# Kernel tuning notes

Hardware: AMD Instinct MI355X
Metric: run time of the kernel (lower is better)

Reference implementation:

```python
import jax, jax.numpy as jnp
import numpy as np

D = 512      # Config.vector_sizes[1]
S = 1024     # Config.sequence_lengths[1]
B = 16       # read batch
Q = 64       # Config.use_pndb1
NDOCS = 8    # external A-matrix memory slots
NL = 2       # encoder layers


def rope(x):
    # rotary position embedding over last dim, x: [b, s, d]
    s, d = x.shape[-2], x.shape[-1]
    inv = 1.0 / (10000.0 ** (jnp.arange(0, d, 2, dtype=jnp.float32) / d))
    ang = jnp.arange(s, dtype=jnp.float32)[:, None] * inv[None, :]  # [s, d/2]
    sin, cos = jnp.sin(ang), jnp.cos(ang)
    x1, x2 = x[..., ::2], x[..., 1::2]
    out = jnp.stack([x1 * cos - x2 * sin, x1 * sin + x2 * cos], axis=-1)
    return out.reshape(x.shape)


def layer_norm(x, g, b):
    m = x.mean(-1, keepdims=True)
    v = ((x - m) ** 2).mean(-1, keepdims=True)
    return (x - m) / jnp.sqrt(v + 1e-5) * g + b


def encoder(x, bias, Wqkv, bqkv, Wo, bo, ln, Wff, bff):
    # post-norm transformer encoder, 1 head, rotary on q/k, additive key bias
    d = x.shape[-1]
    scale = 1.0 / jnp.sqrt(jnp.float32(d))
    for l in range(NL):
        q = rope(x @ Wqkv[l, 0] + bqkv[l, 0])
        k = rope(x @ Wqkv[l, 1] + bqkv[l, 1])
        v = x @ Wqkv[l, 2] + bqkv[l, 2]
        scores = jnp.einsum('bqd,bkd->bqk', q, k) * scale + bias[:, None, :]
        a = jax.nn.softmax(scores, axis=-1)
        o = jnp.einsum('bqk,bkd->bqd', a, v) @ Wo[l] + bo[l]
        x = layer_norm(x + o, ln[l, 0, 0], ln[l, 0, 1])
        f = jax.nn.gelu(x @ Wff[l, 0] + bff[l, 0]) @ Wff[l, 1] + bff[l, 1]
        x = layer_norm(x + f, ln[l, 1, 0], ln[l, 1, 1])
    return x


def setup_inputs() -> dict:
    key = jax.random.key(0)
    ks = jax.random.split(key, 24)
    def n(k, shape, s=0.02):
        return jax.random.normal(k, shape, jnp.float32) * s
    ln_init = jnp.tile(jnp.stack([jnp.ones(D), jnp.zeros(D)]), (NL, 2, 1, 1))  # [NL,2,2,D]
    return {
        'raw_emb': jax.random.normal(ks[0], (NDOCS, S, D), jnp.float32),
        'real_pos_write': jax.random.uniform(ks[1], (NDOCS, S), jnp.float32, 0.05, 0.95),
        'post_dec': jax.random.normal(ks[2], (B, S, D), jnp.float32),
        'real_pos_read': jax.random.uniform(ks[4], (B, S), jnp.float32, 0.05, 0.95),
        'questions': jax.random.uniform(ks[5], (Q, D), jnp.float32),
        'W_k': n(ks[6], (D, D)),
        'W_ig': n(ks[7], (D, 1)), 'b_ig': jnp.zeros((1,)),
        'W_u1': n(ks[8], (D, 1)), 'b_u1': jnp.zeros((1,)),
        'W_u2': n(ks[9], (D, 1)), 'b_u2': jnp.zeros((1,)),
        'b1': jax.random.uniform(ks[10], (1,), jnp.float32),
        'W_ok': n(ks[11], (D, D)), 'b_ok': jnp.zeros((D,)),
        'encw_Wqkv': n(ks[12], (NL, 3, D, D)), 'encw_bqkv': jnp.zeros((NL, 3, D)),
        'encw_Wo': n(ks[13], (NL, D, D)), 'encw_bo': jnp.zeros((NL, D)),
        'encw_ln': ln_init,
        'encw_Wff': n(ks[14], (NL, 2, D, D)), 'encw_bff': jnp.zeros((NL, 2, D)),
        'encr_Wqkv': n(ks[15], (NL, 3, D, D)), 'encr_bqkv': jnp.zeros((NL, 3, D)),
        'encr_Wo': n(ks[16], (NL, D, D)), 'encr_bo': jnp.zeros((NL, D)),
        'encr_ln': ln_init,
        'encr_Wff': n(ks[17], (NL, 2, D, D)), 'encr_bff': jnp.zeros((NL, 2, D)),
        'lookup_ids': jax.random.randint(ks[3], (B,), 0, NDOCS, jnp.int32),
    }


def reference(raw_emb, real_pos_write, post_dec, real_pos_read, questions,
              W_k, W_ig, b_ig, W_u1, b_u1, W_u2, b_u2, b1, W_ok, b_ok,
              encw_Wqkv, encw_bqkv, encw_Wo, encw_bo, encw_ln, encw_Wff, encw_bff,
              encr_Wqkv, encr_bqkv, encr_Wo, encr_bo, encr_ln, encr_Wff, encr_bff,
              lookup_ids):
    # ---- create_A_matrix (write path), one A per document ----
    log_pw = jnp.log(real_pos_write)                       # additive key mask
    k = raw_emb @ W_k                                      # to_k (no bias)
    for_ignore = encoder(raw_emb, log_pw, encw_Wqkv, encw_bqkv, encw_Wo,
                         encw_bo, encw_ln, encw_Wff, encw_bff)
    v = raw_emb * jax.nn.sigmoid(for_ignore @ W_ig + b_ig)  # ignore gate
    scores = jnp.einsum('qd,nsd->nqs', questions, k) / jnp.sqrt(jnp.float32(D))
    scores = scores + log_pw[:, None, :]
    A1s = jnp.einsum('nqs,nsd->nqd', jax.nn.softmax(scores, -1), v)  # [NDOCS,Q,D]

    # ---- get_data_from_A_matrix (read path) ----
    logit_pr = jnp.log(real_pos_read) - jnp.log1p(-real_pos_read)  # prob_to_logit
    for_update = encoder(post_dec, logit_pr, encr_Wqkv, encr_bqkv, encr_Wo,
                         encr_bo, encr_ln, encr_Wff, encr_bff)
    k2 = post_dec @ W_ok + b_ok                            # to_output_k
    selA = A1s[lookup_ids]                                 # index_select gather [B,Q,D]
    a2 = jax.nn.softmax(jnp.einsum('bsd,qd->bsq', k2, questions)
                        / jnp.sqrt(jnp.float32(Q)), -1)
    A2 = jnp.einsum('bsq,bqd->bsd', a2, selA)              # [B,S,D]
    gate = jax.nn.sigmoid(for_update @ W_u1 + b_u1 + A2 @ W_u2 + b_u2 + b1 - 4.0)
    out = post_dec * (1.0 - gate) + A2 * gate
    return out, gate
```

## Files before the change

kernel.cpp:

```cpp
#include <hip/hip_runtime.h>
#include <hip/hip_bf16.h>
#include <math.h>

typedef __attribute__((ext_vector_type(8))) short short8;
typedef __attribute__((ext_vector_type(4))) float f32x4;
typedef unsigned short ushortT;

__device__ __forceinline__ unsigned short f2b(float f) {
  union { float f; unsigned u; } v; v.f = f;
  return (unsigned short)((v.u + 0x7FFFu + ((v.u >> 16) & 1u)) >> 16);
}
__device__ __forceinline__ float b2f(unsigned short h) {
  union { unsigned u; float f; } v; v.u = ((unsigned)h) << 16;
  return v.f;
}
__device__ __forceinline__ float gelu_f(float x) {
  return 0.5f * x * (1.0f + tanhf(0.7978845608028654f * (x + 0.044715f * x * x * x)));
}

__device__ __forceinline__ void async16(ushortT* lds, const ushortT* g) {
  __builtin_amdgcn_global_load_lds(
      (const __attribute__((address_space(1))) void*)g,
      (__attribute__((address_space(3))) void*)lds, 16, 0, 0);
}

template<int EMODE>
__global__ __launch_bounds__(256, 3)
void gemm_f(const ushortT* __restrict__ A, const ushortT* __restrict__ Bt,
            const ushortT* __restrict__ A2, const ushortT* __restrict__ Bt2,
            ushortT* __restrict__ C, ushortT* __restrict__ C2,
            const float* __restrict__ bias, const float* __restrict__ bias2,
            int zsplit, int bmode, float scale, long bstride,
            int K, int lda, int ldb, int ldc,
            long sA, long sB, long sC, const float2* __restrict__ tab)
{
  __shared__ ushortT lds[3][2][128 * 32];
  const int gx = gridDim.x, gy = gridDim.y;
  int flat = blockIdx.x + gx * (blockIdx.y + gy * blockIdx.z);
  const int nwg = gx * gy * gridDim.z;
  if ((nwg & 7) == 0) {
    const int per = nwg >> 3;
    flat = (flat & 7) * per + (flat >> 3);
  }
  const int gxy = gx * gy;
  const int z = flat / gxy;
  const int rem = flat - z * gxy;
  const int bm = (rem / gx) * 128, bn = (rem % gx) * 128;

  int zz = z;
  const ushortT* Ap = A; const ushortT* Bp = Bt; const float* bp = bias;
  if (z >= zsplit) { Ap = A2; Bp = Bt2; bp = bias2; zz = z - zsplit; }
  Ap += (long)zz * sA;
  Bp += (long)zz * sB;
  const long coff = (long)z * sC;
  const int tid = threadIdx.x, wave = tid >> 6, lane = tid & 63;
  const int wm = (wave >> 1) << 6, wn = (wave & 1) << 6;
  const int l15 = lane & 15, quad = lane >> 4;

  const ushortT* gA[2]; const ushortT* gB[2];
  int lchunk[2];
#pragma unroll
  for (int q = 0; q < 2; ++q) {
    int r = 32 * wave + 16 * q + (lane >> 2);
    int sw = (((lane & 3) ^ ((r >> 1) & 3)) << 3);
    gA[q] = Ap + (long)(bm + r) * lda + sw;
    gB[q] = Bp + (long)(bn + r) * ldb + sw;
    lchunk[q] = (wave * 2 + q) * 512;
  }

  f32x4 acc[4][4];
#pragma unroll
  for (int i = 0; i < 4; ++i)
#pragma unroll
    for (int j = 0; j < 4; ++j) acc[i][j] = (f32x4){0.f, 0.f, 0.f, 0.f};

  const int x0 = (l15 >> 1) & 3;
  const int nk = K >> 5;

#pragma unroll
  for (int q = 0; q < 2; ++q) {
    async16(&lds[0][0][lchunk[q]], gA[q]);
    async16(&lds[0][1][lchunk[q]], gB[q]);
  }
#pragma unroll
  for (int q = 0; q < 2; ++q) {
    async16(&lds[1][0][lchunk[q]], gA[q] + 32);
    async16(&lds[1][1][lchunk[q]], gB[q] + 32);
  }

  int rb_ = 0, sb_ = 2;
  for (int k = 0; k < nk; ++k) {
    if (k + 2 < nk) {
      int k0 = (k + 2) << 5;
#pragma unroll
      for (int q = 0; q < 2; ++q) {
        async16(&lds[sb_][0][lchunk[q]], gA[q] + k0);
        async16(&lds[sb_][1][lchunk[q]], gB[q] + k0);
      }
    }
    if (k + 2 < nk)      asm volatile("s_waitcnt vmcnt(8)" ::: "memory");
    else if (k + 1 < nk) asm volatile("s_waitcnt vmcnt(4)" ::: "memory");
    else                 asm volatile("s_waitcnt vmcnt(0)" ::: "memory");
    __builtin_amdgcn_s_barrier();
    asm volatile("" ::: "memory");

    short8 aF[4], bF[4];
#pragma unroll
    for (int t = 0; t < 4; ++t) {
      int ra = (wm + t * 16 + l15) << 5;
      aF[t] = *(const short8*)&lds[rb_][0][ra + ((quad ^ x0) << 3)];
      int rbo = (wn + t * 16 + l15) << 5;
      bF[t] = *(const short8*)&lds[rb_][1][rbo + ((quad ^ x0) << 3)];
    }
#pragma unroll
    for (int i = 0; i < 4; ++i)
#pragma unroll
      for (int j = 0; j < 4; ++j)
        acc[i][j] = __builtin_amdgcn_mfma_f32_16x16x32_bf16(aF[i], bF[j], acc[i][j], 0, 0, 0);

    asm volatile("s_waitcnt lgkmcnt(0)" ::: "memory");
    __builtin_amdgcn_s_barrier();
    asm volatile("" ::: "memory");
    rb_ = (rb_ == 2) ? 0 : rb_ + 1;
    sb_ = (sb_ == 2) ? 0 : sb_ + 1;
  }
  __syncthreads();

  ushortT* ct = &lds[0][0][0];
  const float* bz = bp + (long)zz * bstride;
#pragma unroll
  for (int j = 0; j < 4; ++j) {
    int tcol = wn + j * 16 + l15;
    float cbv = (bmode == 1) ? bz[bn + tcol] : 0.0f;
#pragma unroll
    for (int i = 0; i < 4; ++i) {
      int row0 = wm + i * 16 + (quad << 2);
#pragma unroll
      for (int r = 0; r < 4; ++r) {
        int row = row0 + r;
        float bv = (bmode == 2) ? bz[bm + row] : cbv;
        float v = acc[i][j][r] * scale + bv;
        if (EMODE == 1) v = gelu_f(v);
        ct[(row << 7) + tcol] = f2b(v);
      }
    }
  }
  __syncthreads();

  if (EMODE == 2) {
    const bool isq = (bn < 512);
    ushortT* dbase = isq ? C : C2;
    const int cbase = isq ? bn : bn - 512;
#pragma unroll
    for (int it = 0; it < 8; ++it) {
      int trow = it * 16 + (tid >> 4);
      int tcol = (tid & 15) << 3;
      uint4 u = *(const uint4*)&ct[(trow << 7) + tcol];
      int grow = bm + trow;
      int pos = grow & 1023;
      int pair0 = (cbase + tcol) >> 1;
      const float2* tp = &tab[(pos << 8) + pair0];
      unsigned w[4] = {u.x, u.y, u.z, u.w};
      uint4 o;
      unsigned* op = (unsigned*)&o;
#pragma unroll
      for (int p = 0; p < 4; ++p) {
        float2 sc = tp[p];
        float x1 = b2f((ushortT)(w[p] & 0xFFFFu));
        float x2 = b2f((ushortT)(w[p] >> 16));
        float o1 = x1 * sc.y - x2 * sc.x;
        float o2 = x1 * sc.x + x2 * sc.y;
        op[p] = (unsigned)f2b(o1) | ((unsigned)f2b(o2) << 16);
      }
      *(uint4*)&dbase[coff + (long)grow * 512 + cbase + tcol] = o;
    }
  } else {
#pragma unroll
    for (int it = 0; it < 8; ++it) {
      int trow = it * 16 + (tid >> 4);
      int tcol = (tid & 15) << 3;
      *(uint4*)&C[coff + (long)(bm + trow) * ldc + bn + tcol] =
          *(const uint4*)&ct[(trow << 7) + tcol];
    }
  }
}

__global__ void btrans(const ushortT* __restrict__ in, ushortT* __restrict__ out,
                       int R, int C, long ibs, const int* __restrict__ gather) {
  __shared__ float tile[32][33];
  int z = blockIdx.z;
  long ib = (long)(gather ? gather[z] : z) * ibs;
  long ob = (long)z * (long)R * C;
  int c0 = blockIdx.x << 5, r0 = blockIdx.y << 5;
  int tx = threadIdx.x, ty = threadIdx.y;
#pragma unroll
  for (int dy = 0; dy < 32; dy += 8)
    tile[ty + dy][tx] = b2f(in[ib + (long)(r0 + ty + dy) * C + c0 + tx]);
  __syncthreads();
#pragma unroll
  for (int dy = 0; dy < 32; dy += 8)
    out[ob + (long)(c0 + ty + dy) * R + r0 + tx] = f2b(tile[tx][ty + dy]);
}

struct WSrc { const float* p[8]; int c[8]; };
__global__ void wtrans_all(WSrc ws, ushortT* __restrict__ out) {
  __shared__ float tile[32][33];
  int z = blockIdx.z;
  int g = 0, base = 0;
  while (z - base >= ws.c[g]) { base += ws.c[g]; ++g; }
  const float* src = ws.p[g] + (size_t)(z - base) * 262144;
  ushortT* dst = out + (size_t)z * 262144;
  int c0 = blockIdx.x << 5, r0 = blockIdx.y << 5;
  int tx = threadIdx.x, ty = threadIdx.y;
#pragma unroll
  for (int dy = 0; dy < 32; dy += 8)
    tile[ty + dy][tx] = src[(long)(r0 + ty + dy) * 512 + c0 + tx];
  __syncthreads();
#pragma unroll
  for (int dy = 0; dy < 32; dy += 8)
    dst[(long)(c0 + ty + dy) * 512 + r0 + tx] = f2b(tile[tx][ty + dy]);
}

__device__ __forceinline__ void conv4(const float4* in, uint2* out, long i) {
  float4 v = in[i];
  uint2 r;
  r.x = (unsigned)f2b(v.x) | ((unsigned)f2b(v.y) << 16);
  r.y = (unsigned)f2b(v.z) | ((unsigned)f2b(v.w) << 16);
  out[i] = r;
}
__global__ __launch_bounds__(256)
void setup_k(const float* __restrict__ rpw, const float* __restrict__ rpr,
             const float* __restrict__ questions, const float* __restrict__ raw,
             const float* __restrict__ pd,
             float* __restrict__ pbw, float* __restrict__ pbr, float2* __restrict__ tab,
             uint2* __restrict__ qsb, uint2* __restrict__ rab, uint2* __restrict__ pdb,
             float* __restrict__ zb) {
  int b = blockIdx.x, t = threadIdx.x;
  if (b < 32) { int i = b * 256 + t; float v = rpw[i]; pbw[i] = __logf(v); return; }
  b -= 32;
  if (b < 64) { int i = b * 256 + t; float v = rpr[i]; pbr[i] = __logf(v) - log1pf(-v); return; }
  b -= 64;
  if (b < 1024) {
    float inv = __expf(-(float)t * 0.035977892078032f);
    float s, c;
    sincosf((float)b * inv, &s, &c);
    tab[(b << 8) + t] = make_float2(s, c);
    return;
  }
  b -= 1024;
  if (b < 32) { conv4((const float4*)questions, qsb, (long)b * 256 + t); return; }
  b -= 32;
  if (b < 4096) { conv4((const float4*)raw, rab, (long)b * 256 + t); return; }
  b -= 4096;
  if (b < 8192) { conv4((const float4*)pd, pdb, (long)b * 256 + t); return; }
  b -= 8192;
  zb[b * 256 + t] = 0.0f;
}

__global__ __launch_bounds__(256)
void softmax1024(ushortT* __restrict__ x) {
  int row = blockIdx.x * 4 + (threadIdx.x >> 6), lane = threadIdx.x & 63;
  ushortT* xr = x + (long)row * 1024;
  uint4 u0 = ((const uint4*)xr)[lane * 2];
  uint4 u1 = ((const uint4*)xr)[lane * 2 + 1];
  unsigned w[8] = {u0.x, u0.y, u0.z, u0.w, u1.x, u1.y, u1.z, u1.w};
  float t[16];
#pragma unroll
  for (int i = 0; i < 8; ++i) {
    t[2 * i]     = b2f((ushortT)(w[i] & 0xFFFFu));
    t[2 * i + 1] = b2f((ushortT)(w[i] >> 16));
  }
  float m = t[0];
#pragma unroll
  for (int i = 1; i < 16; ++i) m = fmaxf(m, t[i]);
  for (int o = 32; o; o >>= 1) m = fmaxf(m, __shfl_xor(m, o));
  float s = 0.f;
#pragma unroll
  for (int i = 0; i < 16; ++i) { t[i] = __expf(t[i] - m); s += t[i]; }
  for (int o = 32; o; o >>= 1) s += __shfl_xor(s, o);
  float inv = 1.0f / s;
#pragma unroll
  for (int i = 0; i < 8; ++i)
    w[i] = (unsigned)f2b(t[2 * i] * inv) | ((unsigned)f2b(t[2 * i + 1] * inv) << 16);
  uint4 o0; o0.x = w[0]; o0.y = w[1]; o0.z = w[2]; o0.w = w[3];
  uint4 o1; o1.x = w[4]; o1.y = w[5]; o1.z = w[6]; o1.w = w[7];
  ((uint4*)xr)[lane * 2]     = o0;
  ((uint4*)xr)[lane * 2 + 1] = o1;
}

__global__ __launch_bounds__(256)
void softmax64(ushortT* __restrict__ x, int ldr) {
  int row = blockIdx.x * 4 + (threadIdx.x >> 6), lane = threadIdx.x & 63;
  ushortT* xr = x + (long)row * ldr;
  float t = b2f(xr[lane]);
  float m = t;
  for (int o = 32; o; o >>= 1) m = fmaxf(m, __shfl_xor(m, o));
  float e = __expf(t - m), s = e;
  for (int o = 32; o; o >>= 1) s += __shfl_xor(s, o);
  xr[lane] = f2b(e / s);
}

__global__ __launch_bounds__(256)
void ln_k(const ushortT* __restrict__ src, const ushortT* __restrict__ res,
          const float* __restrict__ gamma, const float* __restrict__ beta,
          const float* __restrict__ gamma2, const float* __restrict__ beta2,
          int rsplit, ushortT* __restrict__ dst) {
  int row = blockIdx.x * 4 + (threadIdx.x >> 6), lane = threadIdx.x & 63;
  const float* gp = gamma; const float* bp = beta;
  if (row >= rsplit) { gp = gamma2; bp = beta2; }
  long off = (long)row * 512 + lane * 8;
  short8 sv = *(const short8*)&src[off];
  short8 rv = *(const short8*)&res[off];
  float a[8]; float s = 0.f, q = 0.f;
#pragma unroll
  for (int j = 0; j < 8; ++j) {
    a[j] = b2f((ushortT)sv[j]) + b2f((ushortT)rv[j]);
    s += a[j]; q += a[j] * a[j];
  }
  for (int o = 32; o; o >>= 1) { s += __shfl_xor(s, o); q += __shfl_xor(q, o); }
  float mean = s * (1.0f / 512.0f);
  float var = q * (1.0f / 512.0f) - mean * mean;
  float rstd = rsqrtf(fmaxf(var, 0.f) + 1e-5f);
  unsigned w[4];
#pragma unroll
  for (int j = 0; j < 4; ++j) {
    float v0 = (a[2 * j]     - mean) * rstd * gp[lane * 8 + 2 * j]     + bp[lane * 8 + 2 * j];
    float v1 = (a[2 * j + 1] - mean) * rstd * gp[lane * 8 + 2 * j + 1] + bp[lane * 8 + 2 * j + 1];
    w[j] = (unsigned)f2b(v0) | ((unsigned)f2b(v1) << 16);
  }
  uint4 o; o.x = w[0]; o.y = w[1]; o.z = w[2]; o.w = w[3];
  *(uint4*)&dst[off] = o;
}

__global__ __launch_bounds__(256)
void gatev_k(const ushortT* __restrict__ fi, const float* __restrict__ raw,
             const float* __restrict__ wig, const float* __restrict__ big,
             ushortT* __restrict__ vout) {
  int row = blockIdx.x * 4 + (threadIdx.x >> 6), lane = threadIdx.x & 63;
  long off = (long)row * 512 + lane * 8;
  short8 fv = *(const short8*)&fi[off];
  float d = 0.f;
#pragma unroll
  for (int j = 0; j < 8; ++j) d += b2f((ushortT)fv[j]) * wig[lane * 8 + j];
  for (int o = 32; o; o >>= 1) d += __shfl_xor(d, o);
  float g = 1.0f / (1.0f + __expf(-(d + big[0])));
  float4 r0 = *(const float4*)&raw[off];
  float4 r1 = *(const float4*)&raw[off + 4];
  unsigned w[4];
  w[0] = (unsigned)f2b(r0.x * g) | ((unsigned)f2b(r0.y * g) << 16);
  w[1] = (unsigned)f2b(r0.z * g) | ((unsigned)f2b(r0.w * g) << 16);
  w[2] = (unsigned)f2b(r1.x * g) | ((unsigned)f2b(r1.y * g) << 16);
  w[3] = (unsigned)f2b(r1.z * g) | ((unsigned)f2b(r1.w * g) << 16);
  uint4 o; o.x = w[0]; o.y = w[1]; o.z = w[2]; o.w = w[3];
  *(uint4*)&vout[off] = o;
}

__global__ __launch_bounds__(256)
void final_k(const ushortT* __restrict__ fu, const ushortT* __restrict__ A2,
             const float* __restrict__ pd, const float* __restrict__ wu1,
             const float* __restrict__ wu2, const float* __restrict__ bu1,
             const float* __restrict__ bu2, const float* __restrict__ b1p,
             float* __restrict__ outx, float* __restrict__ outg) {
  int row = blockIdx.x * 4 + (threadIdx.x >> 6), lane = threadIdx.x & 63;
  long off = (long)row * 512 + lane * 8;
  short8 fv = *(const short8*)&fu[off];
  short8 av = *(const short8*)&A2[off];
  float a2[8]; float d1 = 0.f, d2 = 0.f;
#pragma unroll
  for (int j = 0; j < 8; ++j) {
    a2[j] = b2f((ushortT)av[j]);
    d1 += b2f((ushortT)fv[j]) * wu1[lane * 8 + j];
    d2 += a2[j] * wu2[lane * 8 + j];
  }
  for (int o = 32; o; o >>= 1) { d1 += __shfl_xor(d1, o); d2 += __shfl_xor(d2, o); }
  float g = 1.0f / (1.0f + __expf(-(d1 + d2 + bu1[0] + bu2[0] + b1p[0] - 4.0f)));
  float4 p0 = *(const float4*)&pd[off];
  float4 p1 = *(const float4*)&pd[off + 4];
  float4 o0, o1;
  o0.x = p0.x * (1.0f - g) + a2[0] * g;
  o0.y = p0.y * (1.0f - g) + a2[1] * g;
  o0.z = p0.z * (1.0f - g) + a2[2] * g;
  o0.w = p0.w * (1.0f - g) + a2[3] * g;
  o1.x = p1.x * (1.0f - g) + a2[4] * g;
  o1.y = p1.y * (1.0f - g) + a2[5] * g;
  o1.z = p1.z * (1.0f - g) + a2[6] * g;
  o1.w = p1.w * (1.0f - g) + a2[7] * g;
  *(float4*)&outx[off]     = o0;
  *(float4*)&outx[off + 4] = o1;
  if (lane == 0) outg[row] = g;
}

extern "C" void kernel_launch(void* const* d_in, const int* in_sizes, int n_in,
                              void* d_out, int out_size, void* d_ws, size_t ws_size,
                              hipStream_t stream)
{
  const float* raw_emb = (const float*)d_in[0];
  const float* rpw     = (const float*)d_in[1];
  const float* post_dec= (const float*)d_in[2];
  const float* rpr     = (const float*)d_in[3];
  const float* questions=(const float*)d_in[4];
  const float* W_k  = (const float*)d_in[5];
  const float* W_ig = (const float*)d_in[6];
  const float* b_ig = (const float*)d_in[7];
  const float* W_u1 = (const float*)d_in[8];
  const float* b_u1 = (const float*)d_in[9];
  const float* W_u2 = (const float*)d_in[10];
  const float* b_u2 = (const float*)d_in[11];
  const float* b1   = (const float*)d_in[12];
  const float* W_ok = (const float*)d_in[13];
  const float* b_ok = (const float*)d_in[14];
  const float* ew_qkv = (const float*)d_in[15];
  const float* ew_bqkv= (const float*)d_in[16];
  const float* ew_wo  = (const float*)d_in[17];
  const float* ew_bo  = (const float*)d_in[18];
  const float* ew_ln  = (const float*)d_in[19];
  const float* ew_wff = (const float*)d_in[20];
  const float* ew_bff = (const float*)d_in[21];
  const float* er_qkv = (const float*)d_in[22];
  const float* er_bqkv= (const float*)d_in[23];
  const float* er_wo  = (const float*)d_in[24];
  const float* er_bo  = (const float*)d_in[25];
  const float* er_ln  = (const float*)d_in[26];
  const float* er_wff = (const float*)d_in[27];
  const float* er_bff = (const float*)d_in[28];
  const int* lookup   = (const int*)d_in[29];

  const size_t MAT = 512ull * 512ull;
  const long SD = 1024l * 512;
  const long SZ = 8192l * 512;
  const int BIGZ = 1 << 28;
  char* wsb = (char*)d_ws;
  size_t off = 0;
  auto alloc = [&](size_t b) { char* p = wsb + off; off = (off + b + 255) & ~(size_t)255; return p; };

  ushortT* WT  = (ushortT*)alloc(26 * MAT * 2);
  ushortT* RAB = (ushortT*)alloc(8192ull * 512 * 2);
  ushortT* PDB = (ushortT*)alloc(16384ull * 512 * 2);
  ushortT* XC  = (ushortT*)alloc(24576ull * 512 * 2);
  ushortT* B1  = (ushortT*)alloc(24576ull * 512 * 2);
  ushortT* SC  = (ushortT*)alloc(24ull * 1024 * 1024 * 2);
  ushortT* QB  = (ushortT*)alloc(24576ull * 512 * 2);
  ushortT* KB  = (ushortT*)alloc(24576ull * 512 * 2);
  ushortT* VT  = (ushortT*)alloc(24ull * 512 * 1024 * 2);
  ushortT* KD2 = (ushortT*)alloc(24576ull * 512 * 2);
  ushortT* QSB = (ushortT*)alloc(128ull * 512 * 2);
  ushortT* SC2 = (ushortT*)alloc(16384ull * 128 * 2);
  ushortT* A1S = (ushortT*)alloc(8ull * 128 * 512 * 2);
  ushortT* SAT = (ushortT*)alloc(16ull * 512 * 64 * 2);
  float*   PBW = (float*)alloc(8192 * 4);
  float*   PBR = (float*)alloc(16384 * 4);
  float2*  TAB = (float2*)alloc(1024 * 256 * 8);
  float*   ZB  = (float*)alloc(512 * 4);

  auto gemm = [&](int emode, const ushortT* A, const ushortT* Bt,
                  const ushortT* A2p, const ushortT* Bt2p,
                  ushortT* C, ushortT* C2,
                  const float* bias, const float* bias2, int zsplit,
                  int bmode, float scale, long bstride,
                  int M, int N, int K, int lda, int ldb, int ldc,
                  int Z, long sA, long sB, long sC) {
    dim3 g(N / 128, M / 128, Z);
    if (emode == 0)
      gemm_f<0><<<g, dim3(256), 0, stream>>>(A, Bt, A2p, Bt2p, C, nullptr, bias, bias2,
                                             zsplit, bmode, scale, bstride,
                                             K, lda, ldb, ldc, sA, sB, sC, TAB);
    else if (emode == 1)
      gemm_f<1><<<g, dim3(256), 0, stream>>>(A, Bt, A2p, Bt2p, C, nullptr, bias, bias2,
                                             zsplit, bmode, scale, bstride,
                                             K, lda, ldb, ldc, sA, sB, sC, TAB);
    else
      gemm_f<2><<<g, dim3(256), 0, stream>>>(A, Bt, A2p, Bt2p, C, C2, bias, bias2,
                                             zsplit, bmode, scale, bstride,
                                             K, lda, ldb, ldc, sA, sB, sC, TAB);
  };

  const float isc512 = 0.044194173824159216f;

  WSrc wsrc;
  wsrc.p[0] = W_k;    wsrc.c[0] = 1;
  wsrc.p[1] = W_ok;   wsrc.c[1] = 1;
  wsrc.p[2] = ew_qkv; wsrc.c[2] = 6;
  wsrc.p[3] = ew_wo;  wsrc.c[3] = 2;
  wsrc.p[4] = ew_wff; wsrc.c[4] = 4;
  wsrc.p[5] = er_qkv; wsrc.c[5] = 6;
  wsrc.p[6] = er_wo;  wsrc.c[6] = 2;
  wsrc.p[7] = er_wff; wsrc.c[7] = 4;
  wtrans_all<<<dim3(16, 16, 26), dim3(32, 8), 0, stream>>>(wsrc, WT);
  setup_k<<<13442, 256, 0, stream>>>(rpw, rpr, questions, raw_emb, post_dec,
                                     PBW, PBR, TAB, (uint2*)QSB, (uint2*)RAB, (uint2*)PDB, ZB);

  gemm(0, RAB, WT + 0 * MAT, RAB + SZ, WT + 1 * MAT, KD2, nullptr,
       ZB, b_ok, 1, 1, 1.0f, 0,
       8192, 512, 512, 512, 512, 512, 3, SZ, 0, SZ);

  for (int l = 0; l < 2; ++l) {
    const ushortT* xs = (l == 0) ? RAB : XC;
    const ushortT* WqkW = WT + (size_t)(2 + l * 3) * MAT;
    const ushortT* WqkR = WT + (size_t)(14 + l * 3) * MAT;
    const ushortT* WvW  = WT + (size_t)(4 + l * 3) * MAT;
    const ushortT* WvR  = WT + (size_t)(16 + l * 3) * MAT;
    const ushortT* WoW  = WT + (size_t)(8 + l) * MAT;
    const ushortT* WoR  = WT + (size_t)(20 + l) * MAT;
    const ushortT* Wf0W = WT + (size_t)(10 + l * 2) * MAT;
    const ushortT* Wf0R = WT + (size_t)(22 + l * 2) * MAT;
    const ushortT* Wf1W = WT + (size_t)(11 + l * 2) * MAT;
    const ushortT* Wf1R = WT + (size_t)(23 + l * 2) * MAT;

    gemm(2, xs, WqkW, xs + SZ, WqkR, QB, KB,
         ew_bqkv + (l * 3) * 512, er_bqkv + (l * 3) * 512, 1,
         1, 1.0f, 0,
         8192, 1024, 512, 512, 512, 512, 3, SZ, 0, SZ);
    gemm(0, WvW, xs, WvR, xs + 8 * SD, VT, nullptr,
         ew_bqkv + (l * 3 + 2) * 512, er_bqkv + (l * 3 + 2) * 512, 8,
         2, 1.0f, 0,
         512, 1024, 512, 512, 512, 1024, 24, 0, SD, SD);
    gemm(0, QB, KB, QB, KB, SC, nullptr,
         PBW, PBW, BIGZ, 1, isc512, 1024,
         1024, 1024, 512, 512, 512, 1024, 24, SD, SD, 1024l * 1024);
    softmax1024<<<6144, 256, 0, stream>>>(SC);
    gemm(0, SC, VT, SC, VT, QB, nullptr,
         nullptr, nullptr, BIGZ, 0, 1.0f, 0,
         1024, 512, 1024, 1024, 1024, 512, 24, 1024l * 1024, SD, SD);
    gemm(0, QB, WoW, QB + SZ, WoR, B1, nullptr,
         ew_bo + l * 512, er_bo + l * 512, 1, 1, 1.0f, 0,
         8192, 512, 512, 512, 512, 512, 3, SZ, 0, SZ);
    ln_k<<<6144, 256, 0, stream>>>(xs, B1,
         ew_ln + (l * 4 + 0) * 512, ew_ln + (l * 4 + 1) * 512,
         er_ln + (l * 4 + 0) * 512, er_ln + (l * 4 + 1) * 512, 8192, XC);
    gemm(1, XC, Wf0W, XC + SZ, Wf0R, KB, nullptr,
         ew_bff + (l * 2) * 512, er_bff + (l * 2) * 512, 1, 1, 1.0f, 0,
         8192, 512, 512, 512, 512, 512, 3, SZ, 0, SZ);
    gemm(0, KB, Wf1W, KB + SZ, Wf1R, B1, nullptr,
         ew_bff + (l * 2 + 1) * 512, er_bff + (l * 2 + 1) * 512, 1, 1, 1.0f, 0,
         8192, 512, 512, 512, 512, 512, 3, SZ, 0, SZ);
    ln_k<<<6144, 256, 0, stream>>>(XC, B1,
         ew_ln + (l * 4 + 2) * 512, ew_ln + (l * 4 + 3) * 512,
         er_ln + (l * 4 + 2) * 512, er_ln + (l * 4 + 3) * 512, 8192, XC);
  }

  gatev_k<<<2048, 256, 0, stream>>>(XC, raw_emb, W_ig, b_ig, B1);
  btrans<<<dim3(16, 32, 8), dim3(32, 8), 0, stream>>>(B1, VT, 1024, 512, SD, nullptr);
  gemm(0, QSB, KD2, QSB, KD2, SC2, nullptr,
       PBW, PBW, BIGZ, 1, isc512, 1024,
       128, 1024, 512, 512, 512, 1024, 8, 0, SD, 128l * 1024);
  softmax1024<<<256, 256, 0, stream>>>(SC2);
  gemm(0, SC2, VT, SC2, VT, A1S, nullptr,
       nullptr, nullptr, BIGZ, 0, 1.0f, 0,
       128, 512, 1024, 1024, 1024, 512, 8, 128l * 1024, SD, 128l * 512);

  gemm(0, KD2 + SZ, QSB, KD2 + SZ, QSB, SC2, nullptr,
       nullptr, nullptr, BIGZ, 0, 0.125f, 0,
       16384, 128, 512, 512, 512, 128, 1, 0, 0, 0);
  softmax64<<<4096, 256, 0, stream>>>(SC2, 128);
  btrans<<<dim3(16, 2, 16), dim3(32, 8), 0, stream>>>(A1S, SAT, 64, 512, 128 * 512, lookup);
  gemm(0, SC2, SAT, SC2, SAT, QB, nullptr,
       nullptr, nullptr, BIGZ, 0, 1.0f, 0,
       1024, 512, 64, 128, 64, 512, 16, 1024l * 128, 512l * 64, SD);

  float* outp = (float*)d_out;
  final_k<<<4096, 256, 0, stream>>>(XC + SZ, QB, post_dec, W_u1, W_u2, b_u1, b_u2, b1,
                                    outp, outp + 8388608);
}
```

Before: 806.9 us.

## Add 256x128 eight-wave GEMM kernel for large grids

Adds a new GEMM kernel that uses a 256x128 output tile with 512 threads (8 waves, each computing 64x64) and double-buffered LDS loads. The launcher uses it when M and N are divisible by the tile and the grid still has at least 192 workgroups, and otherwise falls back to the existing 128x128 kernel. The larger tile is meant to raise operand reuse per LDS load and cut global traffic. In exchange it uses fewer workgroups, more LDS, and a two-pass epilogue that stages half of the tile at a time through shared memory.

```diff
diff --git a/kernel.cpp b/kernel.cpp
--- a/kernel.cpp
+++ b/kernel.cpp
@@ -22,6 +22,157 @@
   __builtin_amdgcn_global_load_lds(
       (const __attribute__((address_space(1))) void*)g,
       (__attribute__((address_space(3))) void*)lds, 16, 0, 0);
+}
+
+template<int EMODE>
+__global__ __launch_bounds__(512, 4)
+void gemm8b(const ushortT* __restrict__ A, const ushortT* __restrict__ Bt,
+            const ushortT* __restrict__ A2, const ushortT* __restrict__ Bt2,
+            ushortT* __restrict__ C, ushortT* __restrict__ C2,
+            const float* __restrict__ bias, const float* __restrict__ bias2,
+            int zsplit, int bmode, float scale, long bstride,
+            int K, int lda, int ldb, int ldc,
+            long sA, long sB, long sC, const float2* __restrict__ tab)
+{
+  __shared__ ushortT lds[2][12288];
+  const int gx = gridDim.x, gy = gridDim.y;
+  int flat = blockIdx.x + gx * (blockIdx.y + gy * blockIdx.z);
+  const int nwg = gx * gy * gridDim.z;
+  if ((nwg & 7) == 0) { const int per = nwg >> 3; flat = (flat & 7) * per + (flat >> 3); }
+  const int gxy = gx * gy;
+  const int z = flat / gxy;
+  const int rem = flat - z * gxy;
+  const int bm = (rem / gx) * 256, bn = (rem % gx) * 128;
+
+  int zz = z;
+  const ushortT* Ap = A; const ushortT* Bp = Bt; const float* bp = bias;
+  if (z >= zsplit) { Ap = A2; Bp = Bt2; bp = bias2; zz = z - zsplit; }
+  Ap += (long)zz * sA;
+  Bp += (long)zz * sB;
+  const long coff = (long)z * sC;
+  const int tid = threadIdx.x, wave = tid >> 6, lane = tid & 63;
+  const int wm = (wave >> 1) << 6;
+  const int wn = (wave & 1) << 6;
+  const int l15 = lane & 15, quad = lane >> 4;
+  const int x0 = (l15 >> 1) & 3;
+
+  const ushortT* gA[2]; const ushortT* gBp; int la[2]; int lb;
+#pragma unroll
+  for (int s = 0; s < 2; ++s) {
+    int r = s * 128 + (tid >> 2);
+    int sw = (((tid & 3) ^ ((r >> 1) & 3)) << 3);
+    gA[s] = Ap + (long)(bm + r) * lda + sw;
+    la[s] = s * 4096 + tid * 8;
+  }
+  {
+    int r = tid >> 2;
+    int sw = (((tid & 3) ^ ((r >> 1) & 3)) << 3);
+    gBp = Bp + (long)(bn + r) * ldb + sw;
+    lb = 8192 + tid * 8;
+  }
+
+  f32x4 acc[4][4];
+#pragma unroll
+  for (int i = 0; i < 4; ++i)
+#pragma unroll
+    for (int j = 0; j < 4; ++j) acc[i][j] = (f32x4){0.f, 0.f, 0.f, 0.f};
+
+  const int nk = K >> 5;
+
+  async16(&lds[0][la[0]], gA[0]);
+  async16(&lds[0][la[1]], gA[1]);
+  async16(&lds[0][lb], gBp);
+  asm volatile("s_waitcnt vmcnt(0)" ::: "memory");
+  __builtin_amdgcn_s_barrier();
+
+  int cur = 0;
+  for (int t = 0; t < nk; ++t) {
+    if (t + 1 < nk) {
+      int k0 = (t + 1) << 5;
+      async16(&lds[cur ^ 1][la[0]], gA[0] + k0);
+      async16(&lds[cur ^ 1][la[1]], gA[1] + k0);
+      async16(&lds[cur ^ 1][lb], gBp + k0);
+    }
+    short8 aF[4];
+#pragma unroll
+    for (int i = 0; i < 4; ++i)
+      aF[i] = *(const short8*)&lds[cur][((wm + i * 16 + l15) << 5) + ((quad ^ x0) << 3)];
+#pragma unroll
+    for (int j = 0; j < 4; ++j) {
+      short8 bF = *(const short8*)&lds[cur][8192 + ((wn + j * 16 + l15) << 5) + ((quad ^ x0) << 3)];
+#pragma unroll
+      for (int i = 0; i < 4; ++i)
+        acc[i][j] = __builtin_amdgcn_mfma_f32_16x16x32_bf16(aF[i], bF, acc[i][j], 0, 0, 0);
+    }
+    asm volatile("s_waitcnt vmcnt(0)" ::: "memory");
+    __builtin_amdgcn_s_barrier();
+    cur ^= 1;
+  }
+  __syncthreads();
+
+  ushortT* ct = &lds[0][0];
+  const float* bz = bp + (long)zz * bstride;
+  const int lr = wm & 127;
+  const int myh = wm >> 7;
+#pragma unroll
+  for (int h = 0; h < 2; ++h) {
+    if (myh == h) {
+#pragma unroll
+      for (int j = 0; j < 4; ++j) {
+        int tcol = wn + j * 16 + l15;
+        float cbv = (bmode == 1) ? bz[bn + tcol] : 0.0f;
+#pragma unroll
+        for (int i = 0; i < 4; ++i) {
+          int r0l = lr + i * 16 + (quad << 2);
+#pragma unroll
+          for (int r = 0; r < 4; ++r) {
+            int rowl = r0l + r;
+            float bv = (bmode == 2) ? bz[bm + h * 128 + rowl] : cbv;
+            float v = acc[i][j][r] * scale + bv;
+            if (EMODE == 1) v = gelu_f(v);
+            ct[(rowl << 7) + tcol] = f2b(v);
+          }
+        }
+      }
+    }
+    __syncthreads();
+    if (EMODE == 2) {
+      const bool isq = (bn < 512);
+      ushortT* dbase = isq ? C : C2;
+      const int cbase = isq ? bn : bn - 512;
+#pragma unroll
+      for (int it = 0; it < 4; ++it) {
+        int trow = it * 32 + (tid >> 4);
+        int tcol = (tid & 15) << 3;
+        uint4 u = *(const uint4*)&ct[(trow << 7) + tcol];
+        int grow = bm + h * 128 + trow;
+        int pos = grow & 1023;
+        int pair0 = (cbase + tcol) >> 1;
+        const float2* tp = &tab[(pos << 8) + pair0];
+        unsigned w[4] = {u.x, u.y, u.z, u.w};
+        uint4 o; unsigned* op = (unsigned*)&o;
+#pragma unroll
+        for (int p = 0; p < 4; ++p) {
+          float2 sc = tp[p];
+          float xx1 = b2f((ushortT)(w[p] & 0xFFFFu));
+          float xx2 = b2f((ushortT)(w[p] >> 16));
+          float o1 = xx1 * sc.y - xx2 * sc.x;
+          float o2 = xx1 * sc.x + xx2 * sc.y;
+          op[p] = (unsigned)f2b(o1) | ((unsigned)f2b(o2) << 16);
+        }
+        *(uint4*)&dbase[coff + (long)grow * 512 + cbase + tcol] = o;
+      }
+    } else {
+#pragma unroll
+      for (int it = 0; it < 4; ++it) {
+        int trow = it * 32 + (tid >> 4);
+        int tcol = (tid & 15) << 3;
+        *(uint4*)&C[coff + (long)(bm + h * 128 + trow) * ldc + bn + tcol] =
+            *(const uint4*)&ct[(trow << 7) + tcol];
+      }
+    }
+    __syncthreads();
+  }
 }
 
 template<int EMODE>
@@ -459,19 +610,36 @@
                   int bmode, float scale, long bstride,
                   int M, int N, int K, int lda, int ldb, int ldc,
                   int Z, long sA, long sB, long sC) {
-    dim3 g(N / 128, M / 128, Z);
-    if (emode == 0)
-      gemm_f<0><<<g, dim3(256), 0, stream>>>(A, Bt, A2p, Bt2p, C, nullptr, bias, bias2,
-                                             zsplit, bmode, scale, bstride,
-                                             K, lda, ldb, ldc, sA, sB, sC, TAB);
-    else if (emode == 1)
-      gemm_f<1><<<g, dim3(256), 0, stream>>>(A, Bt, A2p, Bt2p, C, nullptr, bias, bias2,
-                                             zsplit, bmode, scale, bstride,
-                                             K, lda, ldb, ldc, sA, sB, sC, TAB);
-    else
-      gemm_f<2><<<g, dim3(256), 0, stream>>>(A, Bt, A2p, Bt2p, C, C2, bias, bias2,
-                                             zsplit, bmode, scale, bstride,
-                                             K, lda, ldb, ldc, sA, sB, sC, TAB);
+    bool big = (M % 256 == 0) && (N % 128 == 0) && ((M / 256) * (N / 128) * Z >= 192);
+    if (big) {
+      dim3 g(N / 128, M / 256, Z);
+      if (emode == 0)
+        gemm8b<0><<<g, dim3(512), 0, stream>>>(A, Bt, A2p, Bt2p, C, nullptr, bias, bias2,
+                                               zsplit, bmode, scale, bstride,
+                                               K, lda, ldb, ldc, sA, sB, sC, TAB);
+      else if (emode == 1)
+        gemm8b<1><<<g, dim3(512), 0, stream>>>(A, Bt, A2p, Bt2p, C, nullptr, bias, bias2,
+                                               zsplit, bmode, scale, bstride,
+                                               K, lda, ldb, ldc, sA, sB, sC, TAB);
+      else
+        gemm8b<2><<<g, dim3(512), 0, stream>>>(A, Bt, A2p, Bt2p, C, C2, bias, bias2,
+                                               zsplit, bmode, scale, bstride,
+                                               K, lda, ldb, ldc, sA, sB, sC, TAB);
+    } else {
+      dim3 g(N / 128, M / 128, Z);
+      if (emode == 0)
+        gemm_f<0><<<g, dim3(256), 0, stream>>>(A, Bt, A2p, Bt2p, C, nullptr, bias, bias2,
+                                               zsplit, bmode, scale, bstride,
+                                               K, lda, ldb, ldc, sA, sB, sC, TAB);
+      else if (emode == 1)
+        gemm_f<1><<<g, dim3(256), 0, stream>>>(A, Bt, A2p, Bt2p, C, nullptr, bias, bias2,
+                                               zsplit, bmode, scale, bstride,
+                                               K, lda, ldb, ldc, sA, sB, sC, TAB);
+      else
+        gemm_f<2><<<g, dim3(256), 0, stream>>>(A, Bt, A2p, Bt2p, C, C2, bias, bias2,
+                                               zsplit, bmode, scale, bstride,
+                                               K, lda, ldb, ldc, sA, sB, sC, TAB);
+    }
   };
 
   const float isc512 = 0.044194173824159216f;
```

After: 1.069 ms. +32.5%, slower.
